# Performance work log

Measured on AMD Instinct MI355X. Metric: run time of the kernel, lower is better.

Reference implementation:

```python
import jax, jax.numpy as jnp
import numpy as np

B, T, H, L, C = 128, 2048, 256, 2, 7


def _lstm_layer(x, W_ih, W_hh, b_ih, b_hh):
    # x: [B, T, I]; W_ih: [4H, I]; W_hh: [4H, H]
    h_dim = W_hh.shape[1]
    # precompute input contribution for all timesteps
    xg = jnp.einsum('bti,gi->btg', x, W_ih) + b_ih + b_hh  # [B, T, 4H]
    xg_t = jnp.swapaxes(xg, 0, 1)  # [T, B, 4H]

    def step(carry, g_in):
        h, c = carry
        g = g_in + h @ W_hh.T  # [B, 4H]
        i, f, gg, o = jnp.split(g, 4, axis=-1)  # PyTorch gate order i,f,g,o
        i = jax.nn.sigmoid(i)
        f = jax.nn.sigmoid(f)
        gg = jnp.tanh(gg)
        o = jax.nn.sigmoid(o)
        c = f * c + i * gg
        h = o * jnp.tanh(c)
        return (h, c), h

    h0 = jnp.zeros((x.shape[0], h_dim), x.dtype)
    c0 = jnp.zeros((x.shape[0], h_dim), x.dtype)
    _, hs = jax.lax.scan(step, (h0, c0), xg_t)  # [T, B, H]
    return jnp.swapaxes(hs, 0, 1)  # [B, T, H]


def setup_inputs() -> dict:
    key = jax.random.key(0)
    ks = jax.random.split(key, 12)
    s0 = 1.0  # init scale ~ 1/sqrt(H) applied below
    sc = 1.0 / np.sqrt(H)
    inp = {
        'x': jax.random.normal(ks[0], (B, T, 1), dtype=jnp.float32),
        'lengths': jax.random.randint(ks[1], (B,), 1, T + 1, dtype=jnp.int32),
        'W_ih0': jax.random.normal(ks[2], (4 * H, 1), dtype=jnp.float32) * sc,
        'W_hh0': jax.random.normal(ks[3], (4 * H, H), dtype=jnp.float32) * sc,
        'b_ih0': jax.random.normal(ks[4], (4 * H,), dtype=jnp.float32) * sc,
        'b_hh0': jax.random.normal(ks[5], (4 * H,), dtype=jnp.float32) * sc,
        'W_ih1': jax.random.normal(ks[6], (4 * H, H), dtype=jnp.float32) * sc,
        'W_hh1': jax.random.normal(ks[7], (4 * H, H), dtype=jnp.float32) * sc,
        'b_ih1': jax.random.normal(ks[8], (4 * H,), dtype=jnp.float32) * sc,
        'b_hh1': jax.random.normal(ks[9], (4 * H,), dtype=jnp.float32) * sc,
        'W_lin': jax.random.normal(ks[10], (C, H), dtype=jnp.float32) * sc,
        'b_lin': jax.random.normal(ks[11], (C,), dtype=jnp.float32) * sc,
    }
    return inp


def reference(x, lengths, W_ih0, W_hh0, b_ih0, b_hh0, W_ih1, W_hh1, b_ih1, b_hh1, W_lin, b_lin):
    # 2-layer LSTM (batch_first). Padded positions are computed but never read,
    # because the masked mean only covers t < lengths[b] (matches PackedSequence math).
    h1 = _lstm_layer(x, W_ih0, W_hh0, b_ih0, b_hh0)   # [B, T, H]
    h2 = _lstm_layer(h1, W_ih1, W_hh1, b_ih1, b_hh1)  # [B, T, H]
    # per-sample variable-length mean pooling (vectorized segment mean)
    t_idx = jnp.arange(h2.shape[1])
    mask = (t_idx[None, :] < lengths[:, None]).astype(h2.dtype)  # [B, T]
    pooled = jnp.einsum('bth,bt->bh', h2, mask) / lengths[:, None].astype(h2.dtype)
    return pooled @ W_lin.T + b_lin  # [B, C]
```

## Files before the change

### kernel.cpp

```cpp
#include <hip/hip_runtime.h>
#include <stdint.h>

#define TT 2048
#define HH 256
#define BB 128

typedef __attribute__((ext_vector_type(8))) short short8;
typedef __attribute__((ext_vector_type(4))) float f32x4;

__device__ __forceinline__ unsigned short f2bf(float f) {
  union { float f; unsigned int u; } v; v.f = f;
  unsigned int r = v.u + 0x7fffu + ((v.u >> 16) & 1u);
  return (unsigned short)(r >> 16);
}
__device__ __forceinline__ float sigm(float x) { return 1.0f / (1.0f + __expf(-x)); }
__device__ __forceinline__ float tanh_f(float x) { return 1.0f - 2.0f / (1.0f + __expf(2.0f * x)); }

__device__ __forceinline__ void mfma_a(f32x4& acc, short8 a, short8 b) {
  asm("v_mfma_f32_16x16x32_bf16 %0, %1, %2, %0" : "+v"(acc) : "v"(a), "a"(b));
}
__device__ __forceinline__ void mfma_v(f32x4& acc, short8 a, short8 b) {
  asm("v_mfma_f32_16x16x32_bf16 %0, %1, %2, %0" : "+v"(acc) : "v"(a), "v"(b));
}
__device__ __forceinline__ short8 ld16_ic(const unsigned short* p) {
  union { unsigned long long q[2]; short8 v; } u;
  u.q[0] = __hip_atomic_load((const unsigned long long*)p, __ATOMIC_RELAXED, __HIP_MEMORY_SCOPE_AGENT);
  u.q[1] = __hip_atomic_load(((const unsigned long long*)p) + 1, __ATOMIC_RELAXED, __HIP_MEMORY_SCOPE_AGENT);
  return u.v;
}
__device__ __forceinline__ void st2_ic(unsigned short* p, unsigned short v) {
  unsigned int vv = v;
  asm volatile("global_store_short %0, %1, off sc0 sc1" :: "v"(p), "v"(vv) : "memory");
}
__device__ __forceinline__ void vmcnt0() { asm volatile("s_waitcnt vmcnt(0)" ::: "memory"); }
__device__ __forceinline__ void waitN(int* f, int idx, int tgt) {
  for (;;) {
    int v = __hip_atomic_load(&f[idx * 16], __ATOMIC_RELAXED, __HIP_MEMORY_SCOPE_AGENT);
    if (__all(v >= tgt)) break;
    __builtin_amdgcn_s_sleep(1);
  }
}

__global__ void prep_kernel(const float* __restrict__ whh0, const float* __restrict__ wih1,
                            const float* __restrict__ whh1,
                            const float* __restrict__ bih0, const float* __restrict__ bhh0,
                            const float* __restrict__ bih1, const float* __restrict__ bhh1,
                            unsigned short* __restrict__ whh0b, unsigned short* __restrict__ wih1b,
                            unsigned short* __restrict__ whh1b,
                            float* __restrict__ bsum0, float* __restrict__ bsum1,
                            int* __restrict__ flags) {
  int i = blockIdx.x * blockDim.x + threadIdx.x;
  if (i < 262144) {
    whh0b[i] = f2bf(whh0[i]);
    wih1b[i] = f2bf(wih1[i]);
    whh1b[i] = f2bf(whh1[i]);
  }
  if (i < 1024) bsum0[i] = bih0[i] + bhh0[i];
  else if (i < 2048) { int j = i - 1024; bsum1[j] = bih1[j] + bhh1[j]; }
  if (i < 8192) flags[i] = 0;
}

__attribute__((amdgpu_flat_work_group_size(256, 256)))
__attribute__((amdgpu_waves_per_eu(1, 1)))
__global__ void rec_all(
    const float* __restrict__ x,
    const unsigned short* __restrict__ whh0b, const float* __restrict__ wih0,
    const float* __restrict__ bsum0,
    const unsigned short* __restrict__ wih1b,
    const unsigned short* __restrict__ whh1b, const float* __restrict__ bsum1,
    const int* __restrict__ lengths,
    float* __restrict__ pooled,
    unsigned short* __restrict__ h1ring,
    unsigned short* __restrict__ h2ring,
    int* flags)
{
  const int tid = threadIdx.x;
  const int lane = tid & 63;
  const int w = tid >> 6;
  const int l15 = lane & 15, l4 = lane >> 4;
  const int isL1 = (blockIdx.x >= 32);
  const int wg = blockIdx.x & 31;
  const int q = wg >> 3;
  const int bg = wg & 7;
  const int b0 = bg * 16;
  const int unit = q * 64 + w * 16 + l15;
  const int myflag = blockIdx.x;

  const unsigned short* WH = isL1 ? whh1b : whh0b;
  short8 wfh[4][8];
#pragma unroll
  for (int gt = 0; gt < 4; ++gt)
#pragma unroll
    for (int kk = 0; kk < 8; ++kk)
      wfh[gt][kk] = *(const short8*)(WH + (size_t)(gt * 256 + unit) * 256 + kk * 32 + l4 * 8);
  short8 wfi[4][8];
  if (isL1) {
#pragma unroll
    for (int gt = 0; gt < 4; ++gt)
#pragma unroll
      for (int kk = 0; kk < 8; ++kk)
        wfi[gt][kk] = *(const short8*)(wih1b + (size_t)(gt * 256 + unit) * 256 + kk * 32 + l4 * 8);
  }
  float bs_l[4], wih0_l[4];
#pragma unroll
  for (int gt = 0; gt < 4; ++gt) {
    bs_l[gt] = (isL1 ? bsum1 : bsum0)[gt * 256 + unit];
    wih0_l[gt] = isL1 ? 0.0f : wih0[gt * 256 + unit];
  }

  float c_[4] = {0.f, 0.f, 0.f, 0.f};
  float psum[4] = {0.f, 0.f, 0.f, 0.f};
  int len_[4];
#pragma unroll
  for (int r = 0; r < 4; ++r) len_[r] = lengths[b0 + l4 * 4 + r];

  for (int t = 0; t < TT; ++t) {
    {
      int idx = myflag, tgt = 0;
      if (isL1) {
        if (lane < 4) { idx = lane * 8 + bg; tgt = t + 1; }
        else if (lane < 7) { idx = 32 + ((q + (lane - 3)) & 3) * 8 + bg; tgt = t; }
      } else {
        if (lane < 3) { if (t > 0) { idx = ((q + lane + 1) & 3) * 8 + bg; tgt = t; } }
        else if (lane < 7) { idx = 32 + (lane - 3) * 8 + bg;
                             tgt = ((t & 7) == 0 && t >= 8) ? t : 0; }
      }
      waitN(flags, idx, tgt);
    }

    f32x4 z = {0.f, 0.f, 0.f, 0.f};
    f32x4 acc[4];
#pragma unroll
    for (int gt = 0; gt < 4; ++gt) acc[gt] = z;

    if (isL1) {
      const unsigned short* hrow = h1ring + ((size_t)(t & 7) * BB + b0 + l15) * HH;
      short8 af[8];
#pragma unroll
      for (int kk = 0; kk < 8; ++kk) af[kk] = ld16_ic(hrow + kk * 32 + l4 * 8);
#pragma unroll
      for (int gt = 0; gt < 4; ++gt)
#pragma unroll
        for (int kk = 0; kk < 8; ++kk) mfma_v(acc[gt], af[kk], wfi[gt][kk]);
    }
    if (t > 0) {
      const unsigned short* hrow = isL1
          ? h2ring + ((size_t)((t - 1) & 1) * BB + b0 + l15) * HH
          : h1ring + ((size_t)((t - 1) & 7) * BB + b0 + l15) * HH;
      short8 af[8];
#pragma unroll
      for (int kk = 0; kk < 8; ++kk) af[kk] = ld16_ic(hrow + kk * 32 + l4 * 8);
#pragma unroll
      for (int gt = 0; gt < 4; ++gt)
#pragma unroll
        for (int kk = 0; kk < 8; ++kk) mfma_a(acc[gt], af[kk], wfh[gt][kk]);
    }

#pragma unroll
    for (int r = 0; r < 4; ++r) {
      const int sr = l4 * 4 + r;
      const int b = b0 + sr;
      float pre[4];
#pragma unroll
      for (int gt = 0; gt < 4; ++gt) pre[gt] = acc[gt][r] + bs_l[gt];
      if (!isL1) {
        const float xv = x[(size_t)b * TT + t];
#pragma unroll
        for (int gt = 0; gt < 4; ++gt) pre[gt] += xv * wih0_l[gt];
      }
      const float ig = sigm(pre[0]), fg = sigm(pre[1]), gg = tanh_f(pre[2]), og = sigm(pre[3]);
      const float cn = fg * c_[r] + ig * gg;
      c_[r] = cn;
      const float hn = og * tanh_f(cn);
      const unsigned short hb = f2bf(hn);
      if (!isL1) {
        st2_ic(&h1ring[((size_t)(t & 7) * BB + b0 + sr) * HH + unit], hb);
      } else {
        st2_ic(&h2ring[((size_t)(t & 1) * BB + b0 + sr) * HH + unit], hb);
        if (t < len_[r]) psum[r] += hn;
      }
    }
    vmcnt0();
    __syncthreads();
    if (tid == 0)
      __hip_atomic_store(&flags[myflag * 16], t + 1, __ATOMIC_RELAXED, __HIP_MEMORY_SCOPE_AGENT);
  }

  if (isL1) {
#pragma unroll
    for (int r = 0; r < 4; ++r)
      pooled[(size_t)(b0 + l4 * 4 + r) * HH + unit] = psum[r];
  }
}

__global__ void out_kernel(const float* __restrict__ pooled, const int* __restrict__ lengths,
                           const float* __restrict__ wlin, const float* __restrict__ blin,
                           float* __restrict__ out) {
  const int b = blockIdx.x;
  const int lane = threadIdx.x;
  float s[7];
#pragma unroll
  for (int c = 0; c < 7; ++c) s[c] = 0.f;
  for (int k = lane; k < 256; k += 64) {
    const float pv = pooled[b * 256 + k];
#pragma unroll
    for (int c = 0; c < 7; ++c) s[c] += pv * wlin[c * 256 + k];
  }
#pragma unroll
  for (int c = 0; c < 7; ++c) {
#pragma unroll
    for (int off = 32; off > 0; off >>= 1) s[c] += __shfl_down(s[c], off);
  }
  if (lane == 0) {
    const float inv = 1.0f / (float)lengths[b];
#pragma unroll
    for (int c = 0; c < 7; ++c) out[b * 7 + c] = s[c] * inv + blin[c];
  }
}

extern "C" void kernel_launch(void* const* d_in, const int* in_sizes, int n_in,
                              void* d_out, int out_size, void* d_ws, size_t ws_size,
                              hipStream_t stream) {
  const float* x      = (const float*)d_in[0];
  const int*   lengths= (const int*)d_in[1];
  const float* W_ih0  = (const float*)d_in[2];
  const float* W_hh0  = (const float*)d_in[3];
  const float* b_ih0  = (const float*)d_in[4];
  const float* b_hh0  = (const float*)d_in[5];
  const float* W_ih1  = (const float*)d_in[6];
  const float* W_hh1  = (const float*)d_in[7];
  const float* b_ih1  = (const float*)d_in[8];
  const float* b_hh1  = (const float*)d_in[9];
  const float* W_lin  = (const float*)d_in[10];
  const float* b_lin  = (const float*)d_in[11];
  float* out = (float*)d_out;

  char* ws = (char*)d_ws;
  unsigned short* whh0b = (unsigned short*)(ws + 0);
  unsigned short* wih1b = (unsigned short*)(ws + 524288);
  unsigned short* whh1b = (unsigned short*)(ws + 1048576);
  float* bsum0   = (float*)(ws + 1572864);
  float* bsum1   = (float*)(ws + 1576960);
  int*   flags   = (int*)  (ws + 1581056);
  float* pooled  = (float*)(ws + 1613824);
  unsigned short* h2ring = (unsigned short*)(ws + 1744896);
  unsigned short* h1ring = (unsigned short*)(ws + 1875968);

  prep_kernel<<<dim3(1024), dim3(256), 0, stream>>>(
      W_hh0, W_ih1, W_hh1, b_ih0, b_hh0, b_ih1, b_hh1,
      whh0b, wih1b, whh1b, bsum0, bsum1, flags);

  rec_all<<<dim3(64), dim3(256), 0, stream>>>(
      x, whh0b, W_ih0, bsum0, wih1b, whh1b, bsum1, lengths,
      pooled, h1ring, h2ring, flags);

  out_kernel<<<dim3(128), dim3(64), 0, stream>>>(pooled, lengths, W_lin, b_lin, out);
}
```

Baseline: 12.61 ms.

## Replace per-block flag barriers with timestamp-tagged ring entries for fine-grained sync

Each hidden-state value is now stored as a 32-bit word that packs the bf16 value with a 16-bit timestep tag. Consumers poll the ring data directly until every tag matches the expected step, which removes the per-step __syncthreads, the vmcnt drain and the flag stores and loads. The layer-0 ring grows from 8 to 16 slots, and back-pressure on layer 1 is now checked only every 8 steps by reading tags in h2ring. The cost is doubled load and store traffic per element, extra repacking work, and more subtle memory-ordering correctness risks.

```diff
diff --git a/kernel.cpp b/kernel.cpp
--- a/kernel.cpp
+++ b/kernel.cpp
@@ -22,23 +22,21 @@
 __device__ __forceinline__ void mfma_v(f32x4& acc, short8 a, short8 b) {
   asm("v_mfma_f32_16x16x32_bf16 %0, %1, %2, %0" : "+v"(acc) : "v"(a), "v"(b));
 }
-__device__ __forceinline__ short8 ld16_ic(const unsigned short* p) {
-  union { unsigned long long q[2]; short8 v; } u;
-  u.q[0] = __hip_atomic_load((const unsigned long long*)p, __ATOMIC_RELAXED, __HIP_MEMORY_SCOPE_AGENT);
-  u.q[1] = __hip_atomic_load(((const unsigned long long*)p) + 1, __ATOMIC_RELAXED, __HIP_MEMORY_SCOPE_AGENT);
-  return u.v;
-}
-__device__ __forceinline__ void st2_ic(unsigned short* p, unsigned short v) {
-  unsigned int vv = v;
-  asm volatile("global_store_short %0, %1, off sc0 sc1" :: "v"(p), "v"(vv) : "memory");
-}
-__device__ __forceinline__ void vmcnt0() { asm volatile("s_waitcnt vmcnt(0)" ::: "memory"); }
-__device__ __forceinline__ void waitN(int* f, int idx, int tgt) {
-  for (;;) {
-    int v = __hip_atomic_load(&f[idx * 16], __ATOMIC_RELAXED, __HIP_MEMORY_SCOPE_AGENT);
-    if (__all(v >= tgt)) break;
-    __builtin_amdgcn_s_sleep(1);
-  }
+__device__ __forceinline__ unsigned long long ld8_ic(const unsigned int* p) {
+  return __hip_atomic_load((const unsigned long long*)p, __ATOMIC_RELAXED, __HIP_MEMORY_SCOPE_AGENT);
+}
+__device__ __forceinline__ unsigned int ld4_ic(const unsigned int* p) {
+  return __hip_atomic_load(p, __ATOMIC_RELAXED, __HIP_MEMORY_SCOPE_AGENT);
+}
+__device__ __forceinline__ void st4_ic(unsigned int* p, unsigned int v) {
+  __hip_atomic_store(p, v, __ATOMIC_RELAXED, __HIP_MEMORY_SCOPE_AGENT);
+}
+__device__ __forceinline__ short8 pack8(const unsigned long long q[4]) {
+  union { unsigned int u[4]; short8 s; } o;
+#pragma unroll
+  for (int p = 0; p < 4; ++p)
+    o.u[p] = (unsigned int)((q[p] >> 16) & 0xffffull) | (unsigned int)((q[p] >> 48) << 16);
+  return o.s;
 }
 
 __global__ void prep_kernel(const float* __restrict__ whh0, const float* __restrict__ wih1,
@@ -48,7 +46,7 @@
                             unsigned short* __restrict__ whh0b, unsigned short* __restrict__ wih1b,
                             unsigned short* __restrict__ whh1b,
                             float* __restrict__ bsum0, float* __restrict__ bsum1,
-                            int* __restrict__ flags) {
+                            unsigned int* __restrict__ h1ring, unsigned int* __restrict__ h2ring) {
   int i = blockIdx.x * blockDim.x + threadIdx.x;
   if (i < 262144) {
     whh0b[i] = f2bf(whh0[i]);
@@ -57,7 +55,8 @@
   }
   if (i < 1024) bsum0[i] = bih0[i] + bhh0[i];
   else if (i < 2048) { int j = i - 1024; bsum1[j] = bih1[j] + bhh1[j]; }
-  if (i < 8192) flags[i] = 0;
+  h1ring[i] = 0xFFFFFFFFu;
+  if (i < 65536) h2ring[i] = 0xFFFFFFFFu;
 }
 
 __attribute__((amdgpu_flat_work_group_size(256, 256)))
@@ -70,9 +69,8 @@
     const unsigned short* __restrict__ whh1b, const float* __restrict__ bsum1,
     const int* __restrict__ lengths,
     float* __restrict__ pooled,
-    unsigned short* __restrict__ h1ring,
-    unsigned short* __restrict__ h2ring,
-    int* flags)
+    unsigned int* __restrict__ h1ring,
+    unsigned int* __restrict__ h2ring)
 {
   const int tid = threadIdx.x;
   const int lane = tid & 63;
@@ -84,7 +82,6 @@
   const int bg = wg & 7;
   const int b0 = bg * 16;
   const int unit = q * 64 + w * 16 + l15;
-  const int myflag = blockIdx.x;
 
   const unsigned short* WH = isL1 ? whh1b : whh0b;
   short8 wfh[4][8];
@@ -114,76 +111,140 @@
 #pragma unroll
   for (int r = 0; r < 4; ++r) len_[r] = lengths[b0 + l4 * 4 + r];
 
+  const int koff = l4 * 8;
+
   for (int t = 0; t < TT; ++t) {
-    {
-      int idx = myflag, tgt = 0;
-      if (isL1) {
-        if (lane < 4) { idx = lane * 8 + bg; tgt = t + 1; }
-        else if (lane < 7) { idx = 32 + ((q + (lane - 3)) & 3) * 8 + bg; tgt = t; }
-      } else {
-        if (lane < 3) { if (t > 0) { idx = ((q + lane + 1) & 3) * 8 + bg; tgt = t; } }
-        else if (lane < 7) { idx = 32 + (lane - 3) * 8 + bg;
-                             tgt = ((t & 7) == 0 && t >= 8) ? t : 0; }
-      }
-      waitN(flags, idx, tgt);
-    }
-
     f32x4 z = {0.f, 0.f, 0.f, 0.f};
     f32x4 acc[4];
 #pragma unroll
     for (int gt = 0; gt < 4; ++gt) acc[gt] = z;
 
-    if (isL1) {
-      const unsigned short* hrow = h1ring + ((size_t)(t & 7) * BB + b0 + l15) * HH;
-      short8 af[8];
-#pragma unroll
-      for (int kk = 0; kk < 8; ++kk) af[kk] = ld16_ic(hrow + kk * 32 + l4 * 8);
-#pragma unroll
-      for (int gt = 0; gt < 4; ++gt)
-#pragma unroll
-        for (int kk = 0; kk < 8; ++kk) mfma_v(acc[gt], af[kk], wfi[gt][kk]);
+    if (!isL1) {
+      if (t >= 8 && (t & 7) == 0) {
+        const int tm8 = t - 8;
+        const unsigned int* pw = h2ring + ((size_t)(tm8 & 1) * BB + b0) * HH + (lane & 3) * 64;
+        for (;;) {
+          bool ok = true;
+          if (lane < 4) {
+            int e = (int)(short)(ld4_ic(pw) & 0xffffu);
+            ok = (e >= tm8);
+          }
+          if (__all(ok)) break;
+          __builtin_amdgcn_s_sleep(8);
+        }
+      }
+      if (t > 0) {
+        const unsigned int tt = (unsigned int)(t - 1) & 0xffffu;
+        const unsigned int* base = h1ring + ((size_t)((t - 1) & 15) * BB + b0 + l15) * HH;
+        unsigned long long qh[32];
+        for (;;) {
+          bool ok = true;
+#pragma unroll
+          for (int kk = 0; kk < 8; ++kk)
+#pragma unroll
+            for (int p = 0; p < 4; ++p) {
+              unsigned long long v = ld8_ic(base + kk * 32 + koff + p * 2);
+              qh[kk * 4 + p] = v;
+              ok = ok && ((unsigned int)(v & 0xffffull) == tt)
+                      && ((unsigned int)((v >> 32) & 0xffffull) == tt);
+            }
+          if (__all(ok)) break;
+          __builtin_amdgcn_s_sleep(2);
+        }
+        short8 af[8];
+#pragma unroll
+        for (int kk = 0; kk < 8; ++kk) af[kk] = pack8(&qh[kk * 4]);
+#pragma unroll
+        for (int gt = 0; gt < 4; ++gt)
+#pragma unroll
+          for (int kk = 0; kk < 8; ++kk) mfma_a(acc[gt], af[kk], wfh[gt][kk]);
+      }
+#pragma unroll
+      for (int r = 0; r < 4; ++r) {
+        const int sr = l4 * 4 + r;
+        const float xv = x[(size_t)(b0 + sr) * TT + t];
+        float pi = acc[0][r] + bs_l[0] + xv * wih0_l[0];
+        float pf = acc[1][r] + bs_l[1] + xv * wih0_l[1];
+        float pg = acc[2][r] + bs_l[2] + xv * wih0_l[2];
+        float po = acc[3][r] + bs_l[3] + xv * wih0_l[3];
+        const float ig = sigm(pi), fg = sigm(pf), gg = tanh_f(pg), og = sigm(po);
+        const float cn = fg * c_[r] + ig * gg;
+        c_[r] = cn;
+        const float hn = og * tanh_f(cn);
+        const unsigned int word = ((unsigned int)f2bf(hn) << 16) | ((unsigned int)t & 0xffffu);
+        st4_ic(&h1ring[((size_t)(t & 15) * BB + b0 + sr) * HH + unit], word);
+      }
+    } else {
+      short8 af2[8];
+      if (t > 0) {
+        const unsigned int tt = (unsigned int)(t - 1) & 0xffffu;
+        const unsigned int* base = h2ring + ((size_t)((t - 1) & 1) * BB + b0 + l15) * HH;
+        unsigned long long qb[32];
+        for (;;) {
+          bool ok = true;
+#pragma unroll
+          for (int kk = 0; kk < 8; ++kk)
+#pragma unroll
+            for (int p = 0; p < 4; ++p) {
+              unsigned long long v = ld8_ic(base + kk * 32 + koff + p * 2);
+              qb[kk * 4 + p] = v;
+              ok = ok && ((unsigned int)(v & 0xffffull) == tt)
+                      && ((unsigned int)((v >> 32) & 0xffffull) == tt);
+            }
+          if (__all(ok)) break;
+          __builtin_amdgcn_s_sleep(2);
+        }
+#pragma unroll
+        for (int kk = 0; kk < 8; ++kk) af2[kk] = pack8(&qb[kk * 4]);
+      }
+      {
+        const unsigned int tt = (unsigned int)t & 0xffffu;
+        const unsigned int* base = h1ring + ((size_t)(t & 15) * BB + b0 + l15) * HH;
+        unsigned long long qa[32];
+        for (;;) {
+          bool ok = true;
+#pragma unroll
+          for (int kk = 0; kk < 8; ++kk)
+#pragma unroll
+            for (int p = 0; p < 4; ++p) {
+              unsigned long long v = ld8_ic(base + kk * 32 + koff + p * 2);
+              qa[kk * 4 + p] = v;
+              ok = ok && ((unsigned int)(v & 0xffffull) == tt)
+                      && ((unsigned int)((v >> 32) & 0xffffull) == tt);
+            }
+          if (__all(ok)) break;
+          __builtin_amdgcn_s_sleep(2);
+        }
+        short8 af1[8];
+#pragma unroll
+        for (int kk = 0; kk < 8; ++kk) af1[kk] = pack8(&qa[kk * 4]);
+#pragma unroll
+        for (int gt = 0; gt < 4; ++gt)
+#pragma unroll
+          for (int kk = 0; kk < 8; ++kk) mfma_v(acc[gt], af1[kk], wfi[gt][kk]);
+      }
+      if (t > 0) {
+#pragma unroll
+        for (int gt = 0; gt < 4; ++gt)
+#pragma unroll
+          for (int kk = 0; kk < 8; ++kk) mfma_a(acc[gt], af2[kk], wfh[gt][kk]);
+      }
+#pragma unroll
+      for (int r = 0; r < 4; ++r) {
+        const int sr = l4 * 4 + r;
+        float pi = acc[0][r] + bs_l[0];
+        float pf = acc[1][r] + bs_l[1];
+        float pg = acc[2][r] + bs_l[2];
+        float po = acc[3][r] + bs_l[3];
+        const float ig = sigm(pi), fg = sigm(pf), gg = tanh_f(pg), og = sigm(po);
+        const float cn = fg * c_[r] + ig * gg;
+        c_[r] = cn;
+        const float hn = og * tanh_f(cn);
+        const unsigned int word = ((unsigned int)f2bf(hn) << 16) | ((unsigned int)t & 0xffffu);
+        st4_ic(&h2ring[((size_t)(t & 1) * BB + b0 + sr) * HH + unit], word);
+        if (t < len_[r]) psum[r] += hn;
+      }
     }
-    if (t > 0) {
-      const unsigned short* hrow = isL1
-          ? h2ring + ((size_t)((t - 1) & 1) * BB + b0 + l15) * HH
-          : h1ring + ((size_t)((t - 1) & 7) * BB + b0 + l15) * HH;
-      short8 af[8];
-#pragma unroll
-      for (int kk = 0; kk < 8; ++kk) af[kk] = ld16_ic(hrow + kk * 32 + l4 * 8);
-#pragma unroll
-      for (int gt = 0; gt < 4; ++gt)
-#pragma unroll
-        for (int kk = 0; kk < 8; ++kk) mfma_a(acc[gt], af[kk], wfh[gt][kk]);
-    }
-
-#pragma unroll
-    for (int r = 0; r < 4; ++r) {
-      const int sr = l4 * 4 + r;
-      const int b = b0 + sr;
-      float pre[4];
-#pragma unroll
-      for (int gt = 0; gt < 4; ++gt) pre[gt] = acc[gt][r] + bs_l[gt];
-      if (!isL1) {
-        const float xv = x[(size_t)b * TT + t];
-#pragma unroll
-        for (int gt = 0; gt < 4; ++gt) pre[gt] += xv * wih0_l[gt];
-      }
-      const float ig = sigm(pre[0]), fg = sigm(pre[1]), gg = tanh_f(pre[2]), og = sigm(pre[3]);
-      const float cn = fg * c_[r] + ig * gg;
-      c_[r] = cn;
-      const float hn = og * tanh_f(cn);
-      const unsigned short hb = f2bf(hn);
-      if (!isL1) {
-        st2_ic(&h1ring[((size_t)(t & 7) * BB + b0 + sr) * HH + unit], hb);
-      } else {
-        st2_ic(&h2ring[((size_t)(t & 1) * BB + b0 + sr) * HH + unit], hb);
-        if (t < len_[r]) psum[r] += hn;
-      }
-    }
-    vmcnt0();
-    __syncthreads();
-    if (tid == 0)
-      __hip_atomic_store(&flags[myflag * 16], t + 1, __ATOMIC_RELAXED, __HIP_MEMORY_SCOPE_AGENT);
   }
 
   if (isL1) {
@@ -241,18 +302,17 @@
   unsigned short* whh1b = (unsigned short*)(ws + 1048576);
   float* bsum0   = (float*)(ws + 1572864);
   float* bsum1   = (float*)(ws + 1576960);
-  int*   flags   = (int*)  (ws + 1581056);
-  float* pooled  = (float*)(ws + 1613824);
-  unsigned short* h2ring = (unsigned short*)(ws + 1744896);
-  unsigned short* h1ring = (unsigned short*)(ws + 1875968);
-
-  prep_kernel<<<dim3(1024), dim3(256), 0, stream>>>(
+  float* pooled  = (float*)(ws + 1581056);
+  unsigned int* h2ring = (unsigned int*)(ws + 1712128);
+  unsigned int* h1ring = (unsigned int*)(ws + 1974272);
+
+  prep_kernel<<<dim3(2048), dim3(256), 0, stream>>>(
       W_hh0, W_ih1, W_hh1, b_ih0, b_hh0, b_ih1, b_hh1,
-      whh0b, wih1b, whh1b, bsum0, bsum1, flags);
+      whh0b, wih1b, whh1b, bsum0, bsum1, h1ring, h2ring);
 
   rec_all<<<dim3(64), dim3(256), 0, stream>>>(
       x, whh0b, W_ih0, bsum0, wih1b, whh1b, bsum1, lengths,
-      pooled, h1ring, h2ring, flags);
+      pooled, h1ring, h2ring);
 
   out_kernel<<<dim3(128), dim3(64), 0, stream>>>(pooled, lengths, W_lin, b_lin, out);
 }
```

Measured after the change: 23.29 ms. 84.7% more time.

## Replace block barrier with per-wave flags and split layer code paths

Applied to the files above, without the earlier changes.

Each wave now publishes its own progress flag instead of the block syncing with __syncthreads and one thread storing a block flag. Consumers poll sixteen per-wave flags per dependency group rather than one block flag. Layer-0 and layer-1 step bodies are split into separate branches, and layer 1 issues both h1 and h2 fragment loads before its MFMAs. This aims to remove intra-block barrier stalls and let waves proceed independently, at the cost of more flag polling traffic, four times as many flag slots, and the ring-buffer backpressure thresholds change.

```diff
diff --git a/kernel.cpp b/kernel.cpp
--- a/kernel.cpp
+++ b/kernel.cpp
@@ -84,7 +84,7 @@
   const int bg = wg & 7;
   const int b0 = bg * 16;
   const int unit = q * 64 + w * 16 + l15;
-  const int myflag = blockIdx.x;
+  const int myfid = (int)blockIdx.x * 4 + w;
 
   const unsigned short* WH = isL1 ? whh1b : whh0b;
   short8 wfh[4][8];
@@ -116,14 +116,20 @@
 
   for (int t = 0; t < TT; ++t) {
     {
-      int idx = myflag, tgt = 0;
-      if (isL1) {
-        if (lane < 4) { idx = lane * 8 + bg; tgt = t + 1; }
-        else if (lane < 7) { idx = 32 + ((q + (lane - 3)) & 3) * 8 + bg; tgt = t; }
+      int idx = myfid, tgt = 0;
+      if (!isL1) {
+        if (lane < 16) {
+          if (t > 0) { idx = ((lane >> 2) * 8 + bg) * 4 + (lane & 3); tgt = t; }
+        } else if (lane < 32) {
+          if (t >= 8 && (t & 3) == 0) {
+            idx = 128 + (((lane - 16) >> 2) * 8 + bg) * 4 + (lane & 3); tgt = t - 4;
+          }
+        }
       } else {
-        if (lane < 3) { if (t > 0) { idx = ((q + lane + 1) & 3) * 8 + bg; tgt = t; } }
-        else if (lane < 7) { idx = 32 + (lane - 3) * 8 + bg;
-                             tgt = ((t & 7) == 0 && t >= 8) ? t : 0; }
+        if (lane < 16) { idx = ((lane >> 2) * 8 + bg) * 4 + (lane & 3); tgt = t + 1; }
+        else if (lane < 32) {
+          if (t > 0) { idx = 128 + (((lane - 16) >> 2) * 8 + bg) * 4 + (lane & 3); tgt = t; }
+        }
       }
       waitN(flags, idx, tgt);
     }
@@ -133,57 +139,72 @@
 #pragma unroll
     for (int gt = 0; gt < 4; ++gt) acc[gt] = z;
 
-    if (isL1) {
-      const unsigned short* hrow = h1ring + ((size_t)(t & 7) * BB + b0 + l15) * HH;
-      short8 af[8];
-#pragma unroll
-      for (int kk = 0; kk < 8; ++kk) af[kk] = ld16_ic(hrow + kk * 32 + l4 * 8);
+    if (!isL1) {
+      if (t > 0) {
+        const unsigned short* hrow = h1ring + ((size_t)((t - 1) & 7) * BB + b0 + l15) * HH;
+        short8 af[8];
+#pragma unroll
+        for (int kk = 0; kk < 8; ++kk) af[kk] = ld16_ic(hrow + kk * 32 + l4 * 8);
+#pragma unroll
+        for (int gt = 0; gt < 4; ++gt)
+#pragma unroll
+          for (int kk = 0; kk < 8; ++kk) mfma_a(acc[gt], af[kk], wfh[gt][kk]);
+      }
+#pragma unroll
+      for (int r = 0; r < 4; ++r) {
+        const int sr = l4 * 4 + r;
+        const float xv = x[(size_t)(b0 + sr) * TT + t];
+        float pi = acc[0][r] + bs_l[0] + xv * wih0_l[0];
+        float pf = acc[1][r] + bs_l[1] + xv * wih0_l[1];
+        float pg = acc[2][r] + bs_l[2] + xv * wih0_l[2];
+        float po = acc[3][r] + bs_l[3] + xv * wih0_l[3];
+        const float ig = sigm(pi), fg = sigm(pf), gg = tanh_f(pg), og = sigm(po);
+        const float cn = fg * c_[r] + ig * gg;
+        c_[r] = cn;
+        const float hn = og * tanh_f(cn);
+        st2_ic(&h1ring[((size_t)(t & 7) * BB + b0 + sr) * HH + unit], f2bf(hn));
+      }
+    } else {
+      short8 af1[8], af2[8];
+      {
+        const unsigned short* h1row = h1ring + ((size_t)(t & 7) * BB + b0 + l15) * HH;
+#pragma unroll
+        for (int kk = 0; kk < 8; ++kk) af1[kk] = ld16_ic(h1row + kk * 32 + l4 * 8);
+      }
+      if (t > 0) {
+        const unsigned short* h2row = h2ring + ((size_t)((t - 1) & 1) * BB + b0 + l15) * HH;
+#pragma unroll
+        for (int kk = 0; kk < 8; ++kk) af2[kk] = ld16_ic(h2row + kk * 32 + l4 * 8);
+      }
 #pragma unroll
       for (int gt = 0; gt < 4; ++gt)
 #pragma unroll
-        for (int kk = 0; kk < 8; ++kk) mfma_v(acc[gt], af[kk], wfi[gt][kk]);
+        for (int kk = 0; kk < 8; ++kk) mfma_v(acc[gt], af1[kk], wfi[gt][kk]);
+      if (t > 0) {
+#pragma unroll
+        for (int gt = 0; gt < 4; ++gt)
+#pragma unroll
+          for (int kk = 0; kk < 8; ++kk) mfma_a(acc[gt], af2[kk], wfh[gt][kk]);
+      }
+#pragma unroll
+      for (int r = 0; r < 4; ++r) {
+        const int sr = l4 * 4 + r;
+        float pi = acc[0][r] + bs_l[0];
+        float pf = acc[1][r] + bs_l[1];
+        float pg = acc[2][r] + bs_l[2];
+        float po = acc[3][r] + bs_l[3];
+        const float ig = sigm(pi), fg = sigm(pf), gg = tanh_f(pg), og = sigm(po);
+        const float cn = fg * c_[r] + ig * gg;
+        c_[r] = cn;
+        const float hn = og * tanh_f(cn);
+        st2_ic(&h2ring[((size_t)(t & 1) * BB + b0 + sr) * HH + unit], f2bf(hn));
+        if (t < len_[r]) psum[r] += hn;
+      }
     }
-    if (t > 0) {
-      const unsigned short* hrow = isL1
-          ? h2ring + ((size_t)((t - 1) & 1) * BB + b0 + l15) * HH
-          : h1ring + ((size_t)((t - 1) & 7) * BB + b0 + l15) * HH;
-      short8 af[8];
-#pragma unroll
-      for (int kk = 0; kk < 8; ++kk) af[kk] = ld16_ic(hrow + kk * 32 + l4 * 8);
-#pragma unroll
-      for (int gt = 0; gt < 4; ++gt)
-#pragma unroll
-        for (int kk = 0; kk < 8; ++kk) mfma_a(acc[gt], af[kk], wfh[gt][kk]);
-    }
-
-#pragma unroll
-    for (int r = 0; r < 4; ++r) {
-      const int sr = l4 * 4 + r;
-      const int b = b0 + sr;
-      float pre[4];
-#pragma unroll
-      for (int gt = 0; gt < 4; ++gt) pre[gt] = acc[gt][r] + bs_l[gt];
-      if (!isL1) {
-        const float xv = x[(size_t)b * TT + t];
-#pragma unroll
-        for (int gt = 0; gt < 4; ++gt) pre[gt] += xv * wih0_l[gt];
-      }
-      const float ig = sigm(pre[0]), fg = sigm(pre[1]), gg = tanh_f(pre[2]), og = sigm(pre[3]);
-      const float cn = fg * c_[r] + ig * gg;
-      c_[r] = cn;
-      const float hn = og * tanh_f(cn);
-      const unsigned short hb = f2bf(hn);
-      if (!isL1) {
-        st2_ic(&h1ring[((size_t)(t & 7) * BB + b0 + sr) * HH + unit], hb);
-      } else {
-        st2_ic(&h2ring[((size_t)(t & 1) * BB + b0 + sr) * HH + unit], hb);
-        if (t < len_[r]) psum[r] += hn;
-      }
-    }
+
     vmcnt0();
-    __syncthreads();
-    if (tid == 0)
-      __hip_atomic_store(&flags[myflag * 16], t + 1, __ATOMIC_RELAXED, __HIP_MEMORY_SCOPE_AGENT);
+    if (lane == 0)
+      __hip_atomic_store(&flags[myfid * 16], t + 1, __ATOMIC_RELAXED, __HIP_MEMORY_SCOPE_AGENT);
   }
 
   if (isL1) {
```

After: 11.47 ms. 1.1x faster.
